# Performance work log

Hardware: AMD Instinct MI355X
Metric: run time of the kernel (lower is better)

## Reference

```python
import jax, jax.numpy as jnp
import numpy as np

N = 100000
D = 128


def segment_mean(x, idx, n):
    s = jax.ops.segment_sum(x, idx, num_segments=n)
    c = jax.ops.segment_sum(jnp.ones((idx.shape[0],), x.dtype), idx, num_segments=n)
    return s / jnp.maximum(c, 1.0)[:, None]


def setup_inputs() -> dict:
    key = jax.random.key(0)
    ks = jax.random.split(key, 10)
    scale = 1.0 / np.sqrt(D)
    return {
        "embedding": jax.random.normal(ks[0], (N, D), dtype=jnp.float32),
        "W_down": jax.random.normal(ks[1], (D, D), dtype=jnp.float32) * scale,
        "b_down": jnp.zeros((D,), dtype=jnp.float32),
        "W_gcn": jax.random.normal(ks[2], (D, D), dtype=jnp.float32) * scale,
        "b_gcn": jnp.zeros((D,), dtype=jnp.float32),
        "W_up": jax.random.normal(ks[3], (D, D), dtype=jnp.float32) * scale,
        "b_up": jnp.zeros((D,), dtype=jnp.float32),
        "down2up_path": jax.random.randint(ks[4], (2, 100000), 0, N),
        "same_level_edge_index": jax.random.randint(ks[5], (2, 600000), 0, N),
        "up2down_edge_index": jax.random.randint(ks[6], (2, 100000), 0, N),
    }


def _forward(embedding, W_down, b_down, W_gcn, b_gcn, W_up, b_up,
             down2up_path, same_level_edge_index, up2down_edge_index):
    # ---- Down2Up: aggregate children into parents (mean), transform, residual add ----
    src, dst = down2up_path[0], down2up_path[1]
    agg = segment_mean(embedding[src], dst, N)                     # [N, D]
    x = jax.nn.relu(embedding + agg @ W_down + b_down)

    # ---- Same-level GCNConv with self-loops and symmetric normalization ----
    s, d = same_level_edge_index[0], same_level_edge_index[1]
    h = x @ W_gcn                                                  # [N, D]
    deg = jax.ops.segment_sum(jnp.ones((s.shape[0],), h.dtype), d, num_segments=N) + 1.0
    dinv = jax.lax.rsqrt(deg)                                      # deg^{-1/2}
    norm = dinv[s] * dinv[d]                                       # [E]
    x = jax.ops.segment_sum(norm[:, None] * h[s], d, num_segments=N)
    x = x + h * (1.0 / deg)[:, None] + b_gcn                       # self-loop term

    # ---- Up2Down: propagate parents back down to children (mean), transform, residual ----
    src2, dst2 = up2down_edge_index[0], up2down_edge_index[1]
    agg2 = segment_mean(x[src2], dst2, N)
    return jax.nn.relu(x + agg2 @ W_up + b_up)


def reference(embedding, W_down, b_down, W_gcn, b_gcn, W_up, b_up,
              down2up_path, same_level_edge_index, up2down_edge_index):
    return _forward(embedding, W_down, b_down, W_gcn, b_gcn, W_up, b_up,
                    down2up_path, same_level_edge_index, up2down_edge_index)
```

## Files before the change

kernel.cpp:

```cpp
#include <hip/hip_runtime.h>
#include <cstdint>
#include <cstddef>

#define NNODES 100000
#define DIM 128
#define TLD 144

#define NB3   (3 * NNODES)
#define BSH   9
#define NBUCK ((NB3 + 511) >> 9)
#define EPB   2048

typedef unsigned short u16;
typedef uint32_t u32;
typedef __attribute__((ext_vector_type(8))) short v8s;
typedef __attribute__((ext_vector_type(4))) float v4f;

__device__ __forceinline__ float bf2f(u32 u) {
  union { u32 i; float f; } x; x.i = u << 16; return x.f;
}
__device__ __forceinline__ u16 f2bf(float f) {
  union { float f; u32 i; } x; x.f = f;
  u32 r = x.i + 0x7fffu + ((x.i >> 16) & 1u);
  return (u16)(r >> 16);
}
__device__ __forceinline__ u32 packsplit(float f) {
  u16 h = f2bf(f);
  float r = f - bf2f(h);
  u16 l = f2bf(r);
  return (u32)h | ((u32)l << 16);
}

__device__ __forceinline__ size_t pidx(int row, int col) {
  return ((size_t)(row >> 4) << 11) +
         (size_t)(((((row & 3) << 3) + (col >> 4)) << 6) +
                  (((row >> 2) & 3) << 4) + (col & 15));
}


__global__ __launch_bounds__(256) void bin_count(const int* __restrict__ d2u,
    const int* __restrict__ sle, const int* __restrict__ u2d,
    int E1, int E2, int E3, int* __restrict__ bcnt) {
  __shared__ int lc[NBUCK];
  const int tid = threadIdx.x;
  for (int i = tid; i < NBUCK; i += 256) lc[i] = 0;
  __syncthreads();
  const int Etot = E1 + E2 + E3;
  const int base = blockIdx.x * EPB;
#pragma unroll
  for (int k = 0; k < EPB; k += 256) {
    int e = base + k + tid;
    if (e < Etot) {
      int idx;
      if (e < E1)            idx = d2u[E1 + e];
      else if (e < E1 + E2)  idx = NNODES + sle[E2 + (e - E1)];
      else                   idx = 2 * NNODES + u2d[E3 + (e - E1 - E2)];
      atomicAdd(&lc[idx >> BSH], 1);
    }
  }
  __syncthreads();
  for (int i = tid; i < NBUCK; i += 256)
    if (lc[i]) atomicAdd(&bcnt[i], lc[i]);
}

__global__ void bin_scan(const int* __restrict__ bcnt, int* __restrict__ brs,
                         int* __restrict__ bfill) {
  __shared__ int tmp[1024];
  const int tid = threadIdx.x;
  for (int i = tid; i < 1024; i += 256) tmp[i] = (i < NBUCK) ? bcnt[i] : 0;
  __syncthreads();
  for (int off = 1; off < 1024; off <<= 1) {
    int vals[4];
#pragma unroll
    for (int j = 0; j < 4; ++j) { int i = tid + j * 256; vals[j] = (i >= off) ? tmp[i - off] : 0; }
    __syncthreads();
#pragma unroll
    for (int j = 0; j < 4; ++j) { int i = tid + j * 256; tmp[i] += vals[j]; }
    __syncthreads();
  }
  for (int i = tid; i < NBUCK; i += 256) {
    int excl = tmp[i] - bcnt[i];
    brs[i] = excl;
    bfill[i] = excl;
  }
}

__global__ __launch_bounds__(256) void bin_fill(const int* __restrict__ d2u,
    const int* __restrict__ sle, const int* __restrict__ u2d,
    int E1, int E2, int E3, int* __restrict__ bfill, uint2* __restrict__ pairs) {
  __shared__ int lc[NBUCK];
  const int tid = threadIdx.x;
  for (int i = tid; i < NBUCK; i += 256) lc[i] = 0;
  __syncthreads();
  const int Etot = E1 + E2 + E3;
  const int base = blockIdx.x * EPB;
  int vidx[EPB / 256], vsrc[EPB / 256];
#pragma unroll
  for (int k = 0; k < EPB / 256; ++k) {
    int e = base + k * 256 + tid;
    int idx = -1, src = 0;
    if (e < Etot) {
      if (e < E1)            { idx = d2u[E1 + e];                          src = d2u[e]; }
      else if (e < E1 + E2)  { int q = e - E1;      idx = NNODES + sle[E2 + q];      src = sle[q]; }
      else                   { int q = e - E1 - E2; idx = 2 * NNODES + u2d[E3 + q];  src = u2d[q]; }
      atomicAdd(&lc[idx >> BSH], 1);
    }
    vidx[k] = idx; vsrc[k] = src;
  }
  __syncthreads();
  for (int i = tid; i < NBUCK; i += 256) {
    int c = lc[i];
    if (c) lc[i] = atomicAdd(&bfill[i], c);
  }
  __syncthreads();
#pragma unroll
  for (int k = 0; k < EPB / 256; ++k) {
    int idx = vidx[k];
    if (idx >= 0) {
      int pos = atomicAdd(&lc[idx >> BSH], 1);
      pairs[pos] = make_uint2((unsigned)idx, (unsigned)vsrc[k]);
    }
  }
}

__global__ __launch_bounds__(256) void node_count(const uint2* __restrict__ pairs,
    const int* __restrict__ brs, const int* __restrict__ bcnt, int* __restrict__ cnt) {
  __shared__ int c[512];
  const int tid = threadIdx.x;
  const int b = blockIdx.x;
  for (int i = tid; i < 512; i += 256) c[i] = 0;
  __syncthreads();
  const int s = brs[b], m = bcnt[b];
  for (int k = tid; k < m; k += 256) {
    uint2 p = pairs[s + k];
    atomicAdd(&c[p.x & 511], 1);
  }
  __syncthreads();
  const int node0 = b << BSH;
  for (int i = tid; i < 512; i += 256) {
    int g = node0 + i;
    if (g < NB3) cnt[g] = c[i];
  }
}

__global__ __launch_bounds__(256) void scatter_bucket(const uint2* __restrict__ pairs,
    const int* __restrict__ brs, const int* __restrict__ bcnt,
    const int* __restrict__ rs, int* __restrict__ eidx) {
  __shared__ int cur[512];
  const int tid = threadIdx.x;
  const int b = blockIdx.x;
  const int node0 = b << BSH;
  for (int i = tid; i < 512; i += 256) {
    int g = node0 + i;
    cur[i] = (g < NB3) ? rs[g] : 0;
  }
  __syncthreads();
  const int s = brs[b], m = bcnt[b];
  for (int k = tid; k < m; k += 256) {
    uint2 p = pairs[s + k];
    int pos = atomicAdd(&cur[p.x & 511], 1);
    eidx[pos] = (int)p.y;
  }
}


__global__ void scan_blocks(const int* __restrict__ in, int* __restrict__ out,
                            int* __restrict__ bsum, int n) {
  __shared__ int wsum[4];
  const int tid = threadIdx.x;
  const int base = blockIdx.x * 1024 + tid * 4;
  int v0 = 0, v1 = 0, v2 = 0, v3 = 0;
  if (base + 0 < n) v0 = in[base + 0];
  if (base + 1 < n) v1 = in[base + 1];
  if (base + 2 < n) v2 = in[base + 2];
  if (base + 3 < n) v3 = in[base + 3];
  const int tsum = v0 + v1 + v2 + v3;
  const int lane = tid & 63, wid = tid >> 6;
  int x = tsum;
  for (int off = 1; off < 64; off <<= 1) {
    int y = __shfl_up(x, off, 64);
    if (lane >= off) x += y;
  }
  if (lane == 63) wsum[wid] = x;
  __syncthreads();
  int woff = 0;
  for (int w = 0; w < wid; ++w) woff += wsum[w];
  const int excl = woff + x - tsum;
  if (base + 0 < n) out[base + 0] = excl;
  if (base + 1 < n) out[base + 1] = excl + v0;
  if (base + 2 < n) out[base + 2] = excl + v0 + v1;
  if (base + 3 < n) out[base + 3] = excl + v0 + v1 + v2;
  if (tid == 255) bsum[blockIdx.x] = woff + x;
}

__global__ void scan_top(int* __restrict__ bsum, int nb) {
  __shared__ int tmp[1024];
  const int tid = threadIdx.x;
  for (int i = tid; i < 1024; i += 256) tmp[i] = (i < nb) ? bsum[i] : 0;
  __syncthreads();
  for (int off = 1; off < 1024; off <<= 1) {
    int vals[4];
#pragma unroll
    for (int j = 0; j < 4; ++j) { int i = tid + j * 256; vals[j] = (i >= off) ? tmp[i - off] : 0; }
    __syncthreads();
#pragma unroll
    for (int j = 0; j < 4; ++j) { int i = tid + j * 256; tmp[i] += vals[j]; }
    __syncthreads();
  }
  for (int i = tid; i < nb; i += 256) {
    int orig = bsum[i];
    bsum[i] = tmp[i] - orig;
  }
}

__global__ void scan_add(int* __restrict__ out, const int* __restrict__ bsum, int n) {
  const int b = blockIdx.x;
  const int off = bsum[b];
  const int base = b * 1024 + threadIdx.x * 4;
#pragma unroll
  for (int j = 0; j < 4; ++j)
    if (base + j < n) out[base + j] += off;
}

__global__ void make_rnorm(const int* __restrict__ cntB, float* __restrict__ rnorm, int n) {
  int i = blockIdx.x * 256 + threadIdx.x;
  if (i < n) rnorm[i] = rsqrtf((float)cntB[i] + 1.0f);
}

__global__ void make_w_planes(const float* __restrict__ W0, const float* __restrict__ W1,
                              const float* __restrict__ W2,
                              u16* __restrict__ Whi, u16* __restrict__ Wlo) {
  int i = blockIdx.x * 256 + threadIdx.x;
  if (i >= 3 * DIM * DIM) return;
  int j = i & 7, lane = (i >> 3) & 63, ct = (i >> 9) & 7, kk = (i >> 12) & 3, m = i >> 14;
  int lr = lane & 15, quad = lane >> 4;
  int c = ct * 16 + lr;
  int k = kk * 32 + quad * 8 + j;
  const float* W = (m == 0) ? W0 : ((m == 1) ? W1 : W2);
  u32 p = packsplit(W[k * DIM + c]);
  Whi[i] = (u16)(p & 0xffffu);
  Wlo[i] = (u16)(p >> 16);
}


__global__ void gather_gcn(const u16* __restrict__ g,
                           const int* __restrict__ rs, const int* __restrict__ cnt,
                           const int* __restrict__ eidx, const float* __restrict__ rnorm,
                           const float* __restrict__ bias, float* __restrict__ out, int n) {
  int gid = blockIdx.x * 256 + threadIdx.x;
  int i = gid >> 6;
  if (i >= n) return;
  int sub = gid & 63;
  int c = (sub & 31) << 2;
  int start = rs[i], m = cnt[i];
  float4 acc = {0.f, 0.f, 0.f, 0.f};
  if (sub < 32) {
    ushort4 pv = *(const ushort4*)(g + ((size_t)i << 7) + c);
    acc.x = bf2f(pv.x); acc.y = bf2f(pv.y);
    acc.z = bf2f(pv.z); acc.w = bf2f(pv.w);
  }
  int j = sub >> 5;
  for (; j + 2 < m; j += 4) {
    int s0 = eidx[start + j], s1 = eidx[start + j + 2];
    ushort4 p0 = *(const ushort4*)(g + ((size_t)s0 << 7) + c);
    ushort4 p1 = *(const ushort4*)(g + ((size_t)s1 << 7) + c);
    acc.x += bf2f(p0.x) + bf2f(p1.x);
    acc.y += bf2f(p0.y) + bf2f(p1.y);
    acc.z += bf2f(p0.z) + bf2f(p1.z);
    acc.w += bf2f(p0.w) + bf2f(p1.w);
  }
  if (j < m) {
    int s = eidx[start + j];
    ushort4 pv = *(const ushort4*)(g + ((size_t)s << 7) + c);
    acc.x += bf2f(pv.x); acc.y += bf2f(pv.y);
    acc.z += bf2f(pv.z); acc.w += bf2f(pv.w);
  }
  acc.x += __shfl_xor(acc.x, 32);
  acc.y += __shfl_xor(acc.y, 32);
  acc.z += __shfl_xor(acc.z, 32);
  acc.w += __shfl_xor(acc.w, 32);
  if (sub < 32) {
    float ri = rnorm[i];
    float4 bv = *(const float4*)(bias + c);
    float4 o;
    o.x = fmaf(ri, acc.x, bv.x);
    o.y = fmaf(ri, acc.y, bv.y);
    o.z = fmaf(ri, acc.z, bv.z);
    o.w = fmaf(ri, acc.w, bv.w);
    *(float4*)(out + (size_t)i * DIM + c) = o;
  }
}

template<int OUT>
__global__ __launch_bounds__(512) void gather_gemm(
    const float* __restrict__ x,
    const int* __restrict__ rs, const int* __restrict__ cnt,
    const int* __restrict__ eidx,
    const u16* __restrict__ Wgh, const u16* __restrict__ Wgl,
    const float* __restrict__ bias, const float* __restrict__ pre,
    float* outf, u32* opk, int nrows)
{
  __shared__ u16 W[2 * DIM * DIM];
  const int tid = threadIdx.x;
  const int wave = tid >> 6, lane = tid & 63;
  const int lr = lane & 15, quad = lane >> 4;
  const int rowbase = blockIdx.x * 128 + wave * 16;

  int arow = rowbase + lr;
  if (arow >= nrows) arow = nrows - 1;
  const int start = rs[arow], m = cnt[arow];
  float4 fa[4], fb[4];
#pragma unroll
  for (int kk = 0; kk < 4; ++kk) {
    fa[kk] = (float4){0.f, 0.f, 0.f, 0.f};
    fb[kk] = (float4){0.f, 0.f, 0.f, 0.f};
  }
  for (int j = 0; j < m; ++j) {
    int s = eidx[start + j];
    const float* rp = x + (size_t)s * DIM + quad * 8;
#pragma unroll
    for (int kk = 0; kk < 4; ++kk) {
      float4 v0 = *(const float4*)(rp + kk * 32);
      float4 v1 = *(const float4*)(rp + kk * 32 + 4);
      fa[kk].x += v0.x; fa[kk].y += v0.y; fa[kk].z += v0.z; fa[kk].w += v0.w;
      fb[kk].x += v1.x; fb[kk].y += v1.y; fb[kk].z += v1.z; fb[kk].w += v1.w;
    }
  }
  const float inv = 1.0f / fmaxf((float)m, 1.0f);
  v8s afh[4], afl[4];
#pragma unroll
  for (int kk = 0; kk < 4; ++kk) {
    float vs[8] = {fa[kk].x, fa[kk].y, fa[kk].z, fa[kk].w,
                   fb[kk].x, fb[kk].y, fb[kk].z, fb[kk].w};
#pragma unroll
    for (int j = 0; j < 8; ++j) {
      u32 p = packsplit(vs[j] * inv);
      afh[kk][j] = (short)(p & 0xffffu);
      afl[kk][j] = (short)(p >> 16);
    }
  }

  {
    uint4* W4 = (uint4*)W;
    for (int i = tid; i < DIM * DIM / 8; i += 512) {
      W4[i] = ((const uint4*)Wgh)[i];
      W4[DIM * DIM / 8 + i] = ((const uint4*)Wgl)[i];
    }
  }
  __syncthreads();

  v4f acc[8];
#pragma unroll
  for (int ct = 0; ct < 8; ++ct) acc[ct] = (v4f){0.f, 0.f, 0.f, 0.f};

#pragma unroll
  for (int kk = 0; kk < 4; ++kk) {
#pragma unroll
    for (int ct = 0; ct < 8; ++ct) {
      const int wo = ((kk * 8 + ct) << 9) + (lane << 3);
      v8s bh = *(const v8s*)(W + wo);
      v8s bl = *(const v8s*)(W + DIM * DIM + wo);
      acc[ct] = __builtin_amdgcn_mfma_f32_16x16x32_bf16(afh[kk], bh, acc[ct], 0, 0, 0);
      acc[ct] = __builtin_amdgcn_mfma_f32_16x16x32_bf16(afh[kk], bl, acc[ct], 0, 0, 0);
      acc[ct] = __builtin_amdgcn_mfma_f32_16x16x32_bf16(afl[kk], bh, acc[ct], 0, 0, 0);
    }
  }

  if (OUT == 1) {
    const size_t lanebase = ((size_t)(rowbase >> 4) << 11) + quad * 16 + lr;
#pragma unroll
    for (int rg = 0; rg < 4; ++rg) {
      int r = rowbase + quad * 4 + rg;
      if (r < nrows) {
#pragma unroll
        for (int ct = 0; ct < 8; ++ct) {
          const int col = ct * 16 + lr;
          float v = acc[ct][rg] + bias[col] + pre[(size_t)r * DIM + col];
          v = fmaxf(v, 0.f);
          opk[lanebase + (size_t)((rg << 3) + ct) * 64] = packsplit(v);
        }
      }
    }
  } else {
#pragma unroll
    for (int ct = 0; ct < 8; ++ct) {
      const int col = ct * 16 + lr;
      float bv = bias[col];
#pragma unroll
      for (int rg = 0; rg < 4; ++rg) {
        int r = rowbase + quad * 4 + rg;
        if (r < nrows) {
          size_t off = (size_t)r * DIM + col;
          float v = acc[ct][rg] + bv + pre[off];
          outf[off] = fmaxf(v, 0.f);
        }
      }
    }
  }
}

__global__ __launch_bounds__(512) void gemm_b(
    const u32* __restrict__ Apk,
    const u16* __restrict__ Wgh, const u16* __restrict__ Wgl,
    const float* __restrict__ rnorm, u16* __restrict__ obf, int nrows)
{
  __shared__ u16 W[2 * DIM * DIM];
  const int tid = threadIdx.x;
  const int wave = tid >> 6, lane = tid & 63;
  const int lr = lane & 15, quad = lane >> 4;
  const int rowbase = blockIdx.x * 128 + wave * 16;

  int arow = rowbase + lr;
  if (arow >= nrows) arow = nrows - 1;
  uint4 pa[4][2];
#pragma unroll
  for (int kk = 0; kk < 4; ++kk) {
    size_t o = pidx(arow, kk * 32 + quad * 8);
    pa[kk][0] = *(const uint4*)(Apk + o);
    pa[kk][1] = *(const uint4*)(Apk + o + 4);
  }

  {
    uint4* W4 = (uint4*)W;
    for (int i = tid; i < DIM * DIM / 8; i += 512) {
      W4[i] = ((const uint4*)Wgh)[i];
      W4[DIM * DIM / 8 + i] = ((const uint4*)Wgl)[i];
    }
  }
  __syncthreads();

  v8s afh[4], afl[4];
#pragma unroll
  for (int kk = 0; kk < 4; ++kk) {
    u32 u[8] = {pa[kk][0].x, pa[kk][0].y, pa[kk][0].z, pa[kk][0].w,
                pa[kk][1].x, pa[kk][1].y, pa[kk][1].z, pa[kk][1].w};
#pragma unroll
    for (int j = 0; j < 8; ++j) {
      afh[kk][j] = (short)(u[j] & 0xffffu);
      afl[kk][j] = (short)(u[j] >> 16);
    }
  }

  v4f acc[8];
#pragma unroll
  for (int ct = 0; ct < 8; ++ct) acc[ct] = (v4f){0.f, 0.f, 0.f, 0.f};

#pragma unroll
  for (int kk = 0; kk < 4; ++kk) {
#pragma unroll
    for (int ct = 0; ct < 8; ++ct) {
      const int wo = ((kk * 8 + ct) << 9) + (lane << 3);
      v8s bh = *(const v8s*)(W + wo);
      v8s bl = *(const v8s*)(W + DIM * DIM + wo);
      acc[ct] = __builtin_amdgcn_mfma_f32_16x16x32_bf16(afh[kk], bh, acc[ct], 0, 0, 0);
      acc[ct] = __builtin_amdgcn_mfma_f32_16x16x32_bf16(afh[kk], bl, acc[ct], 0, 0, 0);
      acc[ct] = __builtin_amdgcn_mfma_f32_16x16x32_bf16(afl[kk], bh, acc[ct], 0, 0, 0);
    }
  }

  __syncthreads();
  const int lrow0 = wave * 16 + quad * 4;
#pragma unroll
  for (int rg = 0; rg < 4; ++rg) {
    int lrow = lrow0 + rg;
    int r = blockIdx.x * 128 + lrow;
    float sc = rnorm[(r < nrows) ? r : (nrows - 1)];
#pragma unroll
    for (int ct = 0; ct < 8; ++ct) {
      W[lrow * TLD + ct * 16 + lr] = f2bf(acc[ct][rg] * sc);
    }
  }
  __syncthreads();
  const int rowstart = blockIdx.x * 128;
  for (int idx = tid; idx < 128 * 16; idx += 512) {
    int lrow = idx >> 4, c8 = (idx & 15) << 3;
    int r = rowstart + lrow;
    if (r < nrows)
      *(uint4*)(obf + ((size_t)r << 7) + c8) = *(const uint4*)&W[lrow * TLD + c8];
  }
}


extern "C" void kernel_launch(void* const* d_in, const int* in_sizes, int n_in,
                              void* d_out, int out_size, void* d_ws, size_t ws_size,
                              hipStream_t stream) {
  const float* emb = (const float*)d_in[0];
  const float* Wd  = (const float*)d_in[1];
  const float* bd  = (const float*)d_in[2];
  const float* Wg  = (const float*)d_in[3];
  const float* bg  = (const float*)d_in[4];
  const float* Wu  = (const float*)d_in[5];
  const float* bu  = (const float*)d_in[6];
  const int* d2u = (const int*)d_in[7];
  const int* sle = (const int*)d_in[8];
  const int* u2d = (const int*)d_in[9];
  const int E1 = in_sizes[7] / 2;
  const int E2 = in_sizes[8] / 2;
  const int E3 = in_sizes[9] / 2;
  const int Etot = E1 + E2 + E3;
  const int N  = NNODES;
  const size_t nd = (size_t)N * DIM;

  u32* Apk  = (u32*)d_ws;
  u16* Gbf  = (u16*)(Apk + nd);
  int* cnt  = (int*)(Gbf + nd);
  int* bbuf = cnt + 3 * N;
  int* rs   = bbuf + 3 * 1024;
  int* eidx = rs + 3 * N;
  float* rnorm = (float*)(eidx + Etot);
  int* bsum = (int*)(rnorm + N);
  u16* Whi = (u16*)(bsum + 1024);
  u16* Wlo = Whi + 3 * DIM * DIM;
  uint2* pairs = (uint2*)(Wlo + 3 * DIM * DIM);
  int* bcnt  = bbuf;
  int* brs   = bbuf + 1024;
  int* bfill = bbuf + 2048;
  float* xb = (float*)Apk;

  const int gemm_blocks = (N + 127) / 128;
  const int nscan = (3 * N + 1023) / 1024;
  const int ngcn = (N * 64 + 255) / 256;
  const int nbin = (Etot + EPB - 1) / EPB;

  (void)hipMemsetAsync(bcnt, 0, 1024 * sizeof(int), stream);
  make_w_planes<<<(3 * DIM * DIM + 255) / 256, 256, 0, stream>>>(Wd, Wg, Wu, Whi, Wlo);
  bin_count<<<nbin, 256, 0, stream>>>(d2u, sle, u2d, E1, E2, E3, bcnt);
  bin_scan<<<1, 256, 0, stream>>>(bcnt, brs, bfill);
  bin_fill<<<nbin, 256, 0, stream>>>(d2u, sle, u2d, E1, E2, E3, bfill, pairs);
  node_count<<<NBUCK, 256, 0, stream>>>(pairs, brs, bcnt, cnt);
  make_rnorm<<<(N + 255) / 256, 256, 0, stream>>>(cnt + N, rnorm, N);
  scan_blocks<<<nscan, 256, 0, stream>>>(cnt, rs, bsum, 3 * N);
  scan_top<<<1, 256, 0, stream>>>(bsum, nscan);
  scan_add<<<nscan, 256, 0, stream>>>(rs, bsum, 3 * N);
  scatter_bucket<<<NBUCK, 256, 0, stream>>>(pairs, brs, bcnt, rs, eidx);

  gather_gemm<1><<<gemm_blocks, 512, 0, stream>>>(emb, rs, cnt, eidx, Whi, Wlo,
                                                  bd, emb, nullptr, Apk, N);

  gemm_b<<<gemm_blocks, 512, 0, stream>>>(Apk, Whi + DIM * DIM, Wlo + DIM * DIM,
                                          rnorm, Gbf, N);
  gather_gcn<<<ngcn, 256, 0, stream>>>(Gbf, rs + N, cnt + N, eidx, rnorm, bg, xb, N);

  gather_gemm<0><<<gemm_blocks, 512, 0, stream>>>(xb, rs + 2 * N, cnt + 2 * N, eidx,
                                                  Whi + 2 * DIM * DIM, Wlo + 2 * DIM * DIM,
                                                  bu, xb, (float*)d_out, nullptr, N);
}
```

Before: 309.2 us.

## Fuse down-projection and GCN GEMM into one kernel, halve LDS weight staging

The down2up gather+GEMM and the GCN weight GEMM now run in one kernel. The intermediate activation is kept in LDS in the packed hi/lo bf16 layout instead of being written to and reread from global memory, and one launch is removed. Only the high bf16 weight plane is staged in LDS; the low plane is read directly from global memory (through cache) to halve LDS usage, and the up2down kernel gets the same treatment. The cost is global/L2 loads inside the MFMA loop, plus an extra barrier and LDS round trip for the intermediate.

After: 309.7 us. No clear change (+0.2%).

```diff
diff --git a/kernel.cpp b/kernel.cpp
--- a/kernel.cpp
+++ b/kernel.cpp
@@ -29,12 +29,6 @@
   float r = f - bf2f(h);
   u16 l = f2bf(r);
   return (u32)h | ((u32)l << 16);
-}
-
-__device__ __forceinline__ size_t pidx(int row, int col) {
-  return ((size_t)(row >> 4) << 11) +
-         (size_t)(((((row & 3) << 3) + (col >> 4)) << 6) +
-                  (((row >> 2) & 3) << 4) + (col & 15));
 }
 
 
@@ -291,16 +285,16 @@
   }
 }
 
-template<int OUT>
-__global__ __launch_bounds__(512) void gather_gemm(
-    const float* __restrict__ x,
-    const int* __restrict__ rs, const int* __restrict__ cnt,
-    const int* __restrict__ eidx,
+__global__ __launch_bounds__(512) void fused_ab(
+    const float* __restrict__ emb,
+    const int* __restrict__ rs, const int* __restrict__ cnt, const int* __restrict__ eidx,
+    const u16* __restrict__ Wdh, const u16* __restrict__ Wdl,
     const u16* __restrict__ Wgh, const u16* __restrict__ Wgl,
-    const float* __restrict__ bias, const float* __restrict__ pre,
-    float* outf, u32* opk, int nrows)
+    const float* __restrict__ bd, const float* __restrict__ rnorm,
+    u16* __restrict__ obf, int nrows)
 {
-  __shared__ u16 W[2 * DIM * DIM];
+  __shared__ u16 S[2 * DIM * DIM];
+  u32* X = (u32*)S;
   const int tid = threadIdx.x;
   const int wave = tid >> 6, lane = tid & 63;
   const int lr = lane & 15, quad = lane >> 4;
@@ -317,7 +311,7 @@
   }
   for (int j = 0; j < m; ++j) {
     int s = eidx[start + j];
-    const float* rp = x + (size_t)s * DIM + quad * 8;
+    const float* rp = emb + (size_t)s * DIM + quad * 8;
 #pragma unroll
     for (int kk = 0; kk < 4; ++kk) {
       float4 v0 = *(const float4*)(rp + kk * 32);
@@ -341,124 +335,75 @@
   }
 
   {
-    uint4* W4 = (uint4*)W;
-    for (int i = tid; i < DIM * DIM / 8; i += 512) {
-      W4[i] = ((const uint4*)Wgh)[i];
-      W4[DIM * DIM / 8 + i] = ((const uint4*)Wgl)[i];
-    }
+    uint4* W4 = (uint4*)S;
+    for (int i = tid; i < DIM * DIM / 8; i += 512)
+      W4[i] = ((const uint4*)Wdh)[i];
   }
   __syncthreads();
 
   v4f acc[8];
 #pragma unroll
   for (int ct = 0; ct < 8; ++ct) acc[ct] = (v4f){0.f, 0.f, 0.f, 0.f};
-
 #pragma unroll
   for (int kk = 0; kk < 4; ++kk) {
 #pragma unroll
     for (int ct = 0; ct < 8; ++ct) {
       const int wo = ((kk * 8 + ct) << 9) + (lane << 3);
-      v8s bh = *(const v8s*)(W + wo);
-      v8s bl = *(const v8s*)(W + DIM * DIM + wo);
+      v8s bh = *(const v8s*)(S + wo);
+      v8s bl = *(const v8s*)(Wdl + wo);
       acc[ct] = __builtin_amdgcn_mfma_f32_16x16x32_bf16(afh[kk], bh, acc[ct], 0, 0, 0);
       acc[ct] = __builtin_amdgcn_mfma_f32_16x16x32_bf16(afh[kk], bl, acc[ct], 0, 0, 0);
       acc[ct] = __builtin_amdgcn_mfma_f32_16x16x32_bf16(afl[kk], bh, acc[ct], 0, 0, 0);
     }
   }
 
-  if (OUT == 1) {
-    const size_t lanebase = ((size_t)(rowbase >> 4) << 11) + quad * 16 + lr;
-#pragma unroll
-    for (int rg = 0; rg < 4; ++rg) {
-      int r = rowbase + quad * 4 + rg;
-      if (r < nrows) {
-#pragma unroll
-        for (int ct = 0; ct < 8; ++ct) {
-          const int col = ct * 16 + lr;
-          float v = acc[ct][rg] + bias[col] + pre[(size_t)r * DIM + col];
-          v = fmaxf(v, 0.f);
-          opk[lanebase + (size_t)((rg << 3) + ct) * 64] = packsplit(v);
-        }
-      }
-    }
-  } else {
+  __syncthreads();
+
+#pragma unroll
+  for (int rg = 0; rg < 4; ++rg) {
+    int r = rowbase + quad * 4 + rg;
+    int rc = (r < nrows) ? r : (nrows - 1);
 #pragma unroll
     for (int ct = 0; ct < 8; ++ct) {
       const int col = ct * 16 + lr;
-      float bv = bias[col];
-#pragma unroll
-      for (int rg = 0; rg < 4; ++rg) {
-        int r = rowbase + quad * 4 + rg;
-        if (r < nrows) {
-          size_t off = (size_t)r * DIM + col;
-          float v = acc[ct][rg] + bv + pre[off];
-          outf[off] = fmaxf(v, 0.f);
-        }
-      }
-    }
-  }
-}
-
-__global__ __launch_bounds__(512) void gemm_b(
-    const u32* __restrict__ Apk,
-    const u16* __restrict__ Wgh, const u16* __restrict__ Wgl,
-    const float* __restrict__ rnorm, u16* __restrict__ obf, int nrows)
-{
-  __shared__ u16 W[2 * DIM * DIM];
-  const int tid = threadIdx.x;
-  const int wave = tid >> 6, lane = tid & 63;
-  const int lr = lane & 15, quad = lane >> 4;
-  const int rowbase = blockIdx.x * 128 + wave * 16;
-
-  int arow = rowbase + lr;
-  if (arow >= nrows) arow = nrows - 1;
-  uint4 pa[4][2];
-#pragma unroll
-  for (int kk = 0; kk < 4; ++kk) {
-    size_t o = pidx(arow, kk * 32 + quad * 8);
-    pa[kk][0] = *(const uint4*)(Apk + o);
-    pa[kk][1] = *(const uint4*)(Apk + o + 4);
-  }
-
-  {
-    uint4* W4 = (uint4*)W;
-    for (int i = tid; i < DIM * DIM / 8; i += 512) {
-      W4[i] = ((const uint4*)Wgh)[i];
-      W4[DIM * DIM / 8 + i] = ((const uint4*)Wgl)[i];
-    }
-  }
-  __syncthreads();
-
-  v8s afh[4], afl[4];
-#pragma unroll
-  for (int kk = 0; kk < 4; ++kk) {
-    u32 u[8] = {pa[kk][0].x, pa[kk][0].y, pa[kk][0].z, pa[kk][0].w,
-                pa[kk][1].x, pa[kk][1].y, pa[kk][1].z, pa[kk][1].w};
+      float v = acc[ct][rg] + bd[col] + emb[(size_t)rc * DIM + col];
+      v = fmaxf(v, 0.f);
+      X[wave * 2048 + (((rg << 3) + ct) << 6) + (quad << 4) + lr] = packsplit(v);
+    }
+  }
+
+  v8s agh[4], agl[4];
+#pragma unroll
+  for (int kk = 0; kk < 4; ++kk) {
+    const int base = wave * 2048 + ((((lr & 3) << 3) + kk * 2 + (quad >> 1)) << 6) +
+                     (((lr >> 2) & 3) << 4) + ((quad & 1) << 3);
+    uint4 q0 = *(const uint4*)(X + base);
+    uint4 q1 = *(const uint4*)(X + base + 4);
+    u32 u[8] = {q0.x, q0.y, q0.z, q0.w, q1.x, q1.y, q1.z, q1.w};
 #pragma unroll
     for (int j = 0; j < 8; ++j) {
-      afh[kk][j] = (short)(u[j] & 0xffffu);
-      afl[kk][j] = (short)(u[j] >> 16);
-    }
-  }
-
-  v4f acc[8];
+      agh[kk][j] = (short)(u[j] & 0xffffu);
+      agl[kk][j] = (short)(u[j] >> 16);
+    }
+  }
+
 #pragma unroll
   for (int ct = 0; ct < 8; ++ct) acc[ct] = (v4f){0.f, 0.f, 0.f, 0.f};
-
 #pragma unroll
   for (int kk = 0; kk < 4; ++kk) {
 #pragma unroll
     for (int ct = 0; ct < 8; ++ct) {
       const int wo = ((kk * 8 + ct) << 9) + (lane << 3);
-      v8s bh = *(const v8s*)(W + wo);
-      v8s bl = *(const v8s*)(W + DIM * DIM + wo);
-      acc[ct] = __builtin_amdgcn_mfma_f32_16x16x32_bf16(afh[kk], bh, acc[ct], 0, 0, 0);
-      acc[ct] = __builtin_amdgcn_mfma_f32_16x16x32_bf16(afh[kk], bl, acc[ct], 0, 0, 0);
-      acc[ct] = __builtin_amdgcn_mfma_f32_16x16x32_bf16(afl[kk], bh, acc[ct], 0, 0, 0);
-    }
-  }
-
-  __syncthreads();
+      v8s bh = *(const v8s*)(Wgh + wo);
+      v8s bl = *(const v8s*)(Wgl + wo);
+      acc[ct] = __builtin_amdgcn_mfma_f32_16x16x32_bf16(agh[kk], bh, acc[ct], 0, 0, 0);
+      acc[ct] = __builtin_amdgcn_mfma_f32_16x16x32_bf16(agh[kk], bl, acc[ct], 0, 0, 0);
+      acc[ct] = __builtin_amdgcn_mfma_f32_16x16x32_bf16(agl[kk], bh, acc[ct], 0, 0, 0);
+    }
+  }
+
+  __syncthreads();
+
   const int lrow0 = wave * 16 + quad * 4;
 #pragma unroll
   for (int rg = 0; rg < 4; ++rg) {
@@ -467,7 +412,7 @@
     float sc = rnorm[(r < nrows) ? r : (nrows - 1)];
 #pragma unroll
     for (int ct = 0; ct < 8; ++ct) {
-      W[lrow * TLD + ct * 16 + lr] = f2bf(acc[ct][rg] * sc);
+      S[lrow * TLD + ct * 16 + lr] = f2bf(acc[ct][rg] * sc);
     }
   }
   __syncthreads();
@@ -476,7 +421,92 @@
     int lrow = idx >> 4, c8 = (idx & 15) << 3;
     int r = rowstart + lrow;
     if (r < nrows)
-      *(uint4*)(obf + ((size_t)r << 7) + c8) = *(const uint4*)&W[lrow * TLD + c8];
+      *(uint4*)(obf + ((size_t)r << 7) + c8) = *(const uint4*)&S[lrow * TLD + c8];
+  }
+}
+
+__global__ __launch_bounds__(512) void gather_gemm_c(
+    const float* __restrict__ x,
+    const int* __restrict__ rs, const int* __restrict__ cnt, const int* __restrict__ eidx,
+    const u16* __restrict__ Wuh, const u16* __restrict__ Wul,
+    const float* __restrict__ bias, float* __restrict__ outf, int nrows)
+{
+  __shared__ u16 Wh[DIM * DIM];
+  const int tid = threadIdx.x;
+  const int wave = tid >> 6, lane = tid & 63;
+  const int lr = lane & 15, quad = lane >> 4;
+  const int rowbase = blockIdx.x * 128 + wave * 16;
+
+  int arow = rowbase + lr;
+  if (arow >= nrows) arow = nrows - 1;
+  const int start = rs[arow], m = cnt[arow];
+  float4 fa[4], fb[4];
+#pragma unroll
+  for (int kk = 0; kk < 4; ++kk) {
+    fa[kk] = (float4){0.f, 0.f, 0.f, 0.f};
+    fb[kk] = (float4){0.f, 0.f, 0.f, 0.f};
+  }
+  for (int j = 0; j < m; ++j) {
+    int s = eidx[start + j];
+    const float* rp = x + (size_t)s * DIM + quad * 8;
+#pragma unroll
+    for (int kk = 0; kk < 4; ++kk) {
+      float4 v0 = *(const float4*)(rp + kk * 32);
+      float4 v1 = *(const float4*)(rp + kk * 32 + 4);
+      fa[kk].x += v0.x; fa[kk].y += v0.y; fa[kk].z += v0.z; fa[kk].w += v0.w;
+      fb[kk].x += v1.x; fb[kk].y += v1.y; fb[kk].z += v1.z; fb[kk].w += v1.w;
+    }
+  }
+  const float inv = 1.0f / fmaxf((float)m, 1.0f);
+  v8s afh[4], afl[4];
+#pragma unroll
+  for (int kk = 0; kk < 4; ++kk) {
+    float vs[8] = {fa[kk].x, fa[kk].y, fa[kk].z, fa[kk].w,
+                   fb[kk].x, fb[kk].y, fb[kk].z, fb[kk].w};
+#pragma unroll
+    for (int j = 0; j < 8; ++j) {
+      u32 p = packsplit(vs[j] * inv);
+      afh[kk][j] = (short)(p & 0xffffu);
+      afl[kk][j] = (short)(p >> 16);
+    }
+  }
+
+  {
+    uint4* W4 = (uint4*)Wh;
+    for (int i = tid; i < DIM * DIM / 8; i += 512)
+      W4[i] = ((const uint4*)Wuh)[i];
+  }
+  __syncthreads();
+
+  v4f acc[8];
+#pragma unroll
+  for (int ct = 0; ct < 8; ++ct) acc[ct] = (v4f){0.f, 0.f, 0.f, 0.f};
+#pragma unroll
+  for (int kk = 0; kk < 4; ++kk) {
+#pragma unroll
+    for (int ct = 0; ct < 8; ++ct) {
+      const int wo = ((kk * 8 + ct) << 9) + (lane << 3);
+      v8s bh = *(const v8s*)(Wh + wo);
+      v8s bl = *(const v8s*)(Wul + wo);
+      acc[ct] = __builtin_amdgcn_mfma_f32_16x16x32_bf16(afh[kk], bh, acc[ct], 0, 0, 0);
+      acc[ct] = __builtin_amdgcn_mfma_f32_16x16x32_bf16(afh[kk], bl, acc[ct], 0, 0, 0);
+      acc[ct] = __builtin_amdgcn_mfma_f32_16x16x32_bf16(afl[kk], bh, acc[ct], 0, 0, 0);
+    }
+  }
+
+#pragma unroll
+  for (int ct = 0; ct < 8; ++ct) {
+    const int col = ct * 16 + lr;
+    float bv = bias[col];
+#pragma unroll
+    for (int rg = 0; rg < 4; ++rg) {
+      int r = rowbase + quad * 4 + rg;
+      if (r < nrows) {
+        size_t off = (size_t)r * DIM + col;
+        float v = acc[ct][rg] + bv + x[off];
+        outf[off] = fmaxf(v, 0.f);
+      }
+    }
   }
 }
 
@@ -501,8 +531,8 @@
   const int N  = NNODES;
   const size_t nd = (size_t)N * DIM;
 
-  u32* Apk  = (u32*)d_ws;
-  u16* Gbf  = (u16*)(Apk + nd);
+  float* xb = (float*)d_ws;
+  u16* Gbf  = (u16*)(xb + nd);
   int* cnt  = (int*)(Gbf + nd);
   int* bbuf = cnt + 3 * N;
   int* rs   = bbuf + 3 * 1024;
@@ -515,7 +545,6 @@
   int* bcnt  = bbuf;
   int* brs   = bbuf + 1024;
   int* bfill = bbuf + 2048;
-  float* xb = (float*)Apk;
 
   const int gemm_blocks = (N + 127) / 128;
   const int nscan = (3 * N + 1023) / 1024;
@@ -534,14 +563,13 @@
   scan_add<<<nscan, 256, 0, stream>>>(rs, bsum, 3 * N);
   scatter_bucket<<<NBUCK, 256, 0, stream>>>(pairs, brs, bcnt, rs, eidx);
 
-  gather_gemm<1><<<gemm_blocks, 512, 0, stream>>>(emb, rs, cnt, eidx, Whi, Wlo,
-                                                  bd, emb, nullptr, Apk, N);
-
-  gemm_b<<<gemm_blocks, 512, 0, stream>>>(Apk, Whi + DIM * DIM, Wlo + DIM * DIM,
-                                          rnorm, Gbf, N);
+  fused_ab<<<gemm_blocks, 512, 0, stream>>>(emb, rs, cnt, eidx,
+                                            Whi, Wlo, Whi + DIM * DIM, Wlo + DIM * DIM,
+                                            bd, rnorm, Gbf, N);
+
   gather_gcn<<<ngcn, 256, 0, stream>>>(Gbf, rs + N, cnt + N, eidx, rnorm, bg, xb, N);
 
-  gather_gemm<0><<<gemm_blocks, 512, 0, stream>>>(xb, rs + 2 * N, cnt + 2 * N, eidx,
-                                                  Whi + 2 * DIM * DIM, Wlo + 2 * DIM * DIM,
-                                                  bu, xb, (float*)d_out, nullptr, N);
-}
+  gather_gemm_c<<<gemm_blocks, 512, 0, stream>>>(xb, rs + 2 * N, cnt + 2 * N, eidx,
+                                                 Whi + 2 * DIM * DIM, Wlo + 2 * DIM * DIM,
+                                                 bu, (float*)d_out, N);
+}
```
